# Optimization experiments

Measured on AMD Instinct MI355X. Metric: run time of the kernel, lower is better.

The kernel has to match this reference:

```python
import jax, jax.numpy as jnp
import numpy as np

DIM = 512
HEADS = 8
DIM_HEAD = 64
DIM_INNER = HEADS * DIM_HEAD
SCALE = DIM_HEAD ** -0.5


def setup_inputs() -> dict:
    key = jax.random.key(0)
    ks = jax.random.split(key, 8)
    b, n = 2, 1024
    x = jax.random.normal(ks[0], (b, n, DIM), dtype=jnp.float32)
    w = lambda k, i, o: jax.random.normal(k, (i, o), dtype=jnp.float32) * 0.02
    return {
        'x': x,
        'w_q_u': w(ks[1], DIM, DIM_INNER),
        'w_k_u': w(ks[2], DIM, DIM_INNER),
        'w_v_u': w(ks[3], DIM, DIM_INNER),
        'w_q_c': w(ks[4], DIM, DIM_INNER),
        'w_k_c': w(ks[5], DIM, DIM_INNER),
        'w_v_c': w(ks[6], DIM, DIM_INNER),
        'w_out': w(ks[7], DIM_INNER, DIM),
    }


def reference(x, w_q_u, w_k_u, w_v_u, w_q_c, w_k_c, w_v_c, w_out):
    b, n, _ = x.shape

    def proj(w):  # [b,n,dim] -> [b,h,n,d]
        return (x @ w).reshape(b, n, HEADS, DIM_HEAD).transpose(0, 2, 1, 3)

    q_u, k_u, v_u = proj(w_q_u), proj(w_k_u), proj(w_v_u)
    q_c, k_c, v_c = proj(w_q_c), proj(w_k_c), proj(w_v_c)

    idx = jnp.arange(n)
    causal = idx[:, None] >= idx[None, :]  # tril ones (binary causal mask)

    # term1 = (q_c @ v_u^T) * scale, zeroed above diagonal
    term1 = jnp.einsum('bhid,bhjd->bhij', q_c, v_u) * SCALE
    term1 = term1 * causal.astype(term1.dtype)

    # sigmoid term: (q_u @ k_u^T)*scale with lookahead mask tril(-inf, diag=0)
    logits_u = jnp.einsum('bhid,bhjd->bhij', q_u, k_u) * SCALE
    sig = jax.nn.sigmoid(jnp.where(causal, -jnp.inf, logits_u))

    # S_u[i,k] = sum_j term1[i,j] * sig[k,j]
    S_u = jnp.einsum('bhij,bhkj->bhik', term1, sig)

    # S_c: causal-masked QK
    S_c = jnp.einsum('bhid,bhjd->bhij', q_c, k_c) * SCALE
    S_c = jnp.where(causal, S_c, -jnp.inf)

    final_scores = S_c - jax.nn.silu(S_u)
    attn = jax.nn.softmax(final_scores, axis=-1)
    out = jnp.einsum('bhij,bhjd->bhid', attn, v_c)  # [b,h,n,d]
    out = out.transpose(0, 2, 1, 3).reshape(b, n, DIM_INNER)
    return out @ w_out
```

## Files before the change

kernel.cpp:

```cpp
#include <hip/hip_runtime.h>
#include <math.h>


typedef __bf16 bf16x8 __attribute__((ext_vector_type(8)));
typedef float f32x4 __attribute__((ext_vector_type(4)));

#define SCALE 0.125f

#define GLL(g, l) __builtin_amdgcn_global_load_lds(                         \
    (const __attribute__((address_space(1))) void*)(g),                     \
    (__attribute__((address_space(3))) void*)(l), 16, 0, 0)

__device__ __forceinline__ unsigned short f2bf(float f){
  unsigned int x = __builtin_bit_cast(unsigned int, f);
  unsigned int r = (x + 0x7fffu + ((x >> 16) & 1u)) >> 16;
  return (unsigned short)r;
}
__device__ __forceinline__ float bf2f(unsigned short u){
  unsigned int x = ((unsigned int)u) << 16;
  return __builtin_bit_cast(float, x);
}
__device__ __forceinline__ f32x4 mfma16(bf16x8 a, bf16x8 b, f32x4 c){
  return __builtin_amdgcn_mfma_f32_16x16x32_bf16(a, b, c, 0, 0, 0);
}
__device__ __forceinline__ bf16x8 ld8(const unsigned short* p){
  return *(const bf16x8*)p;
}

__device__ const unsigned char QK_CUM[16] =
  {0,1,2,4,6,9,12,16,20,25,30,36,42,49,56,64};

__device__ const unsigned char SC_RB[72] =
  {15,14,11,13,15,10,12,14,15,14,13,12,15,13,11, 9,
   12, 8, 6,15,13,11, 9, 7,15,13,14,10,14,12,10, 8,
    9, 3,14,12,10, 8, 6, 4,15,13,11, 7,11, 9, 7, 5,
   13,10, 8,11, 9, 6, 4, 2,15,14,12, 5, 7, 5, 3, 1,
   14,12,10, 8, 6, 4, 2, 0};
__device__ const unsigned char SC_CT[72] =
  { 1, 1, 0, 1, 2, 0, 1, 2, 0, 0, 0, 0, 3, 2, 1, 0,
    3, 1, 0, 4, 3, 2, 1, 0, 5, 4, 4, 2, 3, 2, 1, 0,
    3, 0, 5, 4, 3, 2, 1, 0, 6, 5, 4, 2, 3, 2, 1, 0,
    6, 4, 3, 5, 4, 2, 1, 0, 7, 6, 5, 1, 3, 2, 1, 0,
    7, 6, 5, 4, 3, 2, 1, 0};

__global__ __launch_bounds__(256) void k_prep(
    const float* __restrict__ x,
    const float* __restrict__ w0, const float* __restrict__ w1,
    const float* __restrict__ w2, const float* __restrict__ w3,
    const float* __restrict__ w4, const float* __restrict__ w5,
    const float* __restrict__ w6,
    unsigned short* __restrict__ xb, unsigned short* __restrict__ wT){
  int t = threadIdx.x;
  if (blockIdx.x < 576){
    for (int i = blockIdx.x * 256 + t; i < 262144; i += 576 * 256){
      float4 v = ((const float4*)x)[i];
      ushort4 o; o.x = f2bf(v.x); o.y = f2bf(v.y); o.z = f2bf(v.z); o.w = f2bf(v.w);
      ((ushort4*)xb)[i] = o;
    }
    return;
  }
  __shared__ float lds[64 * 65];
  int bx = blockIdx.x - 576;
  int mat = bx >> 6, tile = bx & 63, tr = tile >> 3, tc = tile & 7;
  int k0 = tr * 64, c0 = tc * 64;
  const float* src;
  switch (mat){
    case 0: src = w0; break; case 1: src = w1; break; case 2: src = w2; break;
    case 3: src = w3; break; case 4: src = w4; break; case 5: src = w5; break;
    default: src = w6; break;
  }
#pragma unroll
  for (int i = 0; i < 4; ++i){
    int r = (t >> 4) + i * 16, c4 = (t & 15) * 4;
    float4 v = *(const float4*)(src + (size_t)(k0 + r) * 512 + c0 + c4);
    lds[r * 65 + c4 + 0] = v.x; lds[r * 65 + c4 + 1] = v.y;
    lds[r * 65 + c4 + 2] = v.z; lds[r * 65 + c4 + 3] = v.w;
  }
  __syncthreads();
  unsigned short* dst = wT + (size_t)mat * 262144;
#pragma unroll
  for (int i = 0; i < 4; ++i){
    int oc = (t >> 4) + i * 16;
    int kq = (t & 15) * 4;
    ushort4 o;
    o.x = f2bf(lds[(kq + 0) * 65 + oc]);
    o.y = f2bf(lds[(kq + 1) * 65 + oc]);
    o.z = f2bf(lds[(kq + 2) * 65 + oc]);
    o.w = f2bf(lds[(kq + 3) * 65 + oc]);
    *(ushort4*)(dst + (size_t)(c0 + oc) * 512 + k0 + kq) = o;
  }
}

__global__ __launch_bounds__(256) void k_proj(
    const unsigned short* __restrict__ xb, const unsigned short* __restrict__ wT,
    unsigned short* __restrict__ P){
  __shared__ __align__(16) unsigned short sA[2 * 2 * 64 * 32];
  __shared__ __align__(16) unsigned short sB[2 * 2 * 128 * 32];
  int t = threadIdx.x, lane = t & 63, l16 = lane & 15, quad = lane >> 4;
  int w = t >> 6, wm = w >> 1, wn = w & 1;
  int bx = blockIdx.x;
  int mt = bx / 24, nt = bx - mt * 24;
  int M0 = mt * 64, N0 = nt * 128;
  int matb = N0 >> 9;
  int nin = N0 & 511;
  int srow = (lane >> 2), scol = (lane & 3) * 8;
  const unsigned short* gA = xb + (size_t)(M0 + w*16 + srow) * 512 + scol;
  const unsigned short* gB = wT + (size_t)matb * 262144
                               + (size_t)(nin + w*32 + srow) * 512 + scol;
  unsigned short* lA = sA + (w*16) * 32;
  unsigned short* lB = sB + (w*32) * 32;
  f32x4 acc[4][2] = {};
#define STAGE_PROJ(buf, k0) do {                                   \
    GLL(gA + (k0),               lA + (buf)*4096);                 \
    GLL(gB + (k0),               lB + (buf)*8192);                 \
    GLL(gB + (k0) + 16*512,      lB + (buf)*8192 + 16*32);         \
    GLL(gA + (k0) + 32,          lA + (buf)*4096 + 2048);          \
    GLL(gB + (k0) + 32,          lB + (buf)*8192 + 4096);          \
    GLL(gB + (k0) + 32 + 16*512, lB + (buf)*8192 + 4096 + 16*32);  \
  } while(0)
  STAGE_PROJ(0, 0);
  for (int it = 0; it < 8; ++it){
    if (it < 7){
      STAGE_PROJ((it+1) & 1, (it+1)*64);
      asm volatile("s_waitcnt vmcnt(6)" ::: "memory");
    } else {
      asm volatile("s_waitcnt vmcnt(0)" ::: "memory");
    }
    __builtin_amdgcn_s_barrier();
    int b = it & 1;
#pragma unroll
    for (int h = 0; h < 2; ++h){
      bf16x8 aw[4], ax[2];
#pragma unroll
      for (int fi = 0; fi < 4; ++fi)
        aw[fi] = *(const bf16x8*)(sB + b*8192 + h*4096 + (wn*64 + fi*16 + l16) * 32 + quad * 8);
#pragma unroll
      for (int mi = 0; mi < 2; ++mi)
        ax[mi] = *(const bf16x8*)(sA + b*4096 + h*2048 + (wm*32 + mi*16 + l16) * 32 + quad * 8);
#pragma unroll
      for (int fi = 0; fi < 4; ++fi)
#pragma unroll
        for (int mi = 0; mi < 2; ++mi)
          acc[fi][mi] = mfma16(aw[fi], ax[mi], acc[fi][mi]);
    }
    __builtin_amdgcn_s_barrier();
  }
#undef STAGE_PROJ
#pragma unroll
  for (int fi = 0; fi < 4; ++fi)
#pragma unroll
    for (int mi = 0; mi < 2; ++mi){
      int row = M0 + wm*32 + mi*16 + l16;
      int b_ = row >> 10, n_ = row & 1023;
      int c0 = N0 + wn*64 + fi*16 + quad*4;
      int h = (c0 & 511) >> 6, d = c0 & 63;
      int bh = b_*8 + h;
      ushort4 o;
      o.x = f2bf(acc[fi][mi][0]); o.y = f2bf(acc[fi][mi][1]);
      o.z = f2bf(acc[fi][mi][2]); o.w = f2bf(acc[fi][mi][3]);
      *(ushort4*)(P + (size_t)(matb*16 + bh) * 65536 + (size_t)n_ * 64 + d) = o;
    }
}

__global__ __launch_bounds__(256) void k_qk_vct(
    const unsigned short* __restrict__ P,
    unsigned short* __restrict__ term1, unsigned short* __restrict__ sig,
    unsigned short* __restrict__ vcT){
  int t = threadIdx.x;
  if (blockIdx.x < 256){
    __shared__ unsigned short lds[64 * 72];
    int bh = blockIdx.x >> 4, nt = blockIdx.x & 15;
    int N0 = nt * 64;
    const unsigned short* src = P + (size_t)(5*16 + bh) * 65536 + (size_t)N0 * 64;
#pragma unroll
    for (int i2 = 0; i2 < 2; ++i2){
      int id = i2 * 256 + t;
      int r = id >> 3, c8 = (id & 7) * 8;
      ushort4 v0 = *(const ushort4*)(src + r * 64 + c8);
      ushort4 v1 = *(const ushort4*)(src + r * 64 + c8 + 4);
      *(ushort4*)(lds + r * 72 + c8) = v0;
      *(ushort4*)(lds + r * 72 + c8 + 4) = v1;
    }
    __syncthreads();
    unsigned short* dst = vcT + (size_t)bh * 65536;
#pragma unroll
    for (int i2 = 0; i2 < 2; ++i2){
      int id = i2 * 256 + t;
      int dd = id >> 3, n8 = (id & 7) * 8;
      ushort4 a, b;
      a.x = lds[(n8+0)*72 + dd]; a.y = lds[(n8+1)*72 + dd];
      a.z = lds[(n8+2)*72 + dd]; a.w = lds[(n8+3)*72 + dd];
      b.x = lds[(n8+4)*72 + dd]; b.y = lds[(n8+5)*72 + dd];
      b.z = lds[(n8+6)*72 + dd]; b.w = lds[(n8+7)*72 + dd];
      *(ushort4*)(dst + (size_t)dd * 1024 + N0 + n8) = a;
      *(ushort4*)(dst + (size_t)dd * 1024 + N0 + n8 + 4) = b;
    }
    return;
  }
  __shared__ unsigned short sA[2 * 64 * 32], sB[2 * 128 * 32];
  int id = blockIdx.x - 256;
  int bh = id & 15, tt = id >> 4;
  int mat = (tt >= 72);
  int tl = mat ? tt - 72 : tt;
  int rb = 15;
  while (QK_CUM[rb] > tl) --rb;
  int ct = tl - QK_CUM[rb];
  int R0, C0;
  const unsigned short *Asrc, *Bsrc;
  if (!mat){ R0 = rb * 64;        C0 = ct * 128;
             Asrc = P + (size_t)(3*16 + bh) * 65536;
             Bsrc = P + (size_t)(2*16 + bh) * 65536; }
  else     { R0 = (15 - rb) * 64; C0 = (7 - ct) * 128;
             Asrc = P + (size_t)(0*16 + bh) * 65536;
             Bsrc = P + (size_t)(1*16 + bh) * 65536; }
  int lane = t & 63, l16 = lane & 15, quad = lane >> 4;
  int w = t >> 6, wm = w >> 1, wn = w & 1;
  int srow = lane >> 2, scol = (lane & 3) * 8;
  const unsigned short* gA = Asrc + (size_t)(R0 + w*16 + srow) * 64 + scol;
  const unsigned short* gB = Bsrc + (size_t)(C0 + w*32 + srow) * 64 + scol;
  unsigned short* lA0 = sA + (w*16) * 32;
  unsigned short* lB0 = sB + (w*32) * 32;
  unsigned short* lA1 = lA0 + 64 * 32;
  unsigned short* lB1 = lB0 + 128 * 32;
  f32x4 acc[4][2] = {};
  GLL(gA,              lA0);
  GLL(gB,              lB0);
  GLL(gB + 16*64,      lB0 + 16*32);
  GLL(gA + 32,         lA1);
  GLL(gB + 32,         lB1);
  GLL(gB + 32 + 16*64, lB1 + 16*32);
  __syncthreads();
#pragma unroll
  for (int h = 0; h < 2; ++h){
    bf16x8 af[2], bfr[4];
#pragma unroll
    for (int mi = 0; mi < 2; ++mi)
      af[mi] = *(const bf16x8*)(sA + h*2048 + (wm*32 + mi*16 + l16) * 32 + quad * 8);
#pragma unroll
    for (int fi = 0; fi < 4; ++fi)
      bfr[fi] = *(const bf16x8*)(sB + h*4096 + (wn*64 + fi*16 + l16) * 32 + quad * 8);
#pragma unroll
    for (int fi = 0; fi < 4; ++fi)
#pragma unroll
      for (int mi = 0; mi < 2; ++mi)
        acc[fi][mi] = mfma16(bfr[fi], af[mi], acc[fi][mi]);
  }
  unsigned short* out = (mat ? sig : term1) + (size_t)bh * 1048576;
#pragma unroll
  for (int fi = 0; fi < 4; ++fi)
#pragma unroll
    for (int mi = 0; mi < 2; ++mi){
      int row = R0 + wm*32 + mi*16 + l16;
      int c0 = C0 + wn*64 + fi*16 + quad*4;
      ushort4 o;
#pragma unroll
      for (int r = 0; r < 4; ++r){
        int col = c0 + r;
        float v = acc[fi][mi][r] * SCALE;
        unsigned short res;
        if (!mat) res = (col <= row) ? f2bf(v) : (unsigned short)0;
        else      res = (col >  row) ? f2bf(1.f / (1.f + expf(-v))) : (unsigned short)0;
        ((unsigned short*)&o)[r] = res;
      }
      *(ushort4*)(out + (size_t)row * 1024 + c0) = o;
    }
}

__global__ __launch_bounds__(256) void k_flash(
    const unsigned short* __restrict__ P,
    const unsigned short* __restrict__ term1,
    const unsigned short* __restrict__ sig,
    const unsigned short* __restrict__ vcT,
    float* __restrict__ Opart, float* __restrict__ MS){
  __shared__ __align__(16) unsigned short smem[2*64*32 + 2*128*32];
  unsigned short* sA = smem;
  unsigned short* sB = smem + 4096;
  unsigned short* probs = smem;
  float* red = (float*)smem;
  __shared__ float wpm[2][64], wps[2][64];
  int t = threadIdx.x;
  int bh = blockIdx.x & 15, tt = blockIdx.x >> 4;
  int rb = SC_RB[tt], ct = SC_CT[tt];
  int R0 = rb * 64, C0 = ct * 128;
  int n_it = rb + 1 - 2*ct;
  size_t sbase = (size_t)bh * 1048576;
  int lane = t & 63, l16 = lane & 15, quad = lane >> 4, w = t >> 6;
  int wm = w >> 1, wn = w & 1;
  int srow = lane >> 2, scol = (lane & 3) * 8;
  unsigned short* lA0 = sA + (w*16) * 32;
  unsigned short* lB0 = sB + (w*32) * 32;
  unsigned short* lA1 = lA0 + 2048;
  unsigned short* lB1 = lB0 + 4096;
  const unsigned short* Qc = P + (size_t)(3*16 + bh) * 65536;
  const unsigned short* Kc = P + (size_t)(4*16 + bh) * 65536;
  const unsigned short* Vt = vcT + (size_t)bh * 65536;
  const unsigned short* gA = term1 + sbase + (size_t)(R0 + w*16 + srow) * 1024 + scol;
  const unsigned short* gB = sig   + sbase + (size_t)(C0 + w*32 + srow) * 1024 + scol;
  f32x4 acc_u[4][2] = {};
  for (int it = 0; it < n_it; ++it){
    int j0 = C0 + it * 64;
    GLL(gA + j0,                lA0);
    GLL(gB + j0,                lB0);
    GLL(gB + j0 + 16*1024,      lB0 + 16*32);
    GLL(gA + j0 + 32,           lA1);
    GLL(gB + j0 + 32,           lB1);
    GLL(gB + j0 + 32 + 16*1024, lB1 + 16*32);
    __syncthreads();
#pragma unroll
    for (int h = 0; h < 2; ++h){
      bf16x8 af[2], bfr[4];
#pragma unroll
      for (int mi = 0; mi < 2; ++mi)
        af[mi] = *(const bf16x8*)(sA + h*2048 + (wm*32 + mi*16 + l16) * 32 + quad * 8);
#pragma unroll
      for (int fi = 0; fi < 4; ++fi)
        bfr[fi] = *(const bf16x8*)(sB + h*4096 + (wn*64 + fi*16 + l16) * 32 + quad * 8);
#pragma unroll
      for (int fi = 0; fi < 4; ++fi)
#pragma unroll
        for (int mi = 0; mi < 2; ++mi)
          acc_u[fi][mi] = mfma16(bfr[fi], af[mi], acc_u[fi][mi]);
    }
    __syncthreads();
  }
  f32x4 acc_c[4][2] = {};
#pragma unroll
  for (int kk = 0; kk < 2; ++kk){
    bf16x8 aqk[2], bfr[4];
#pragma unroll
    for (int mi = 0; mi < 2; ++mi)
      aqk[mi] = ld8(Qc + (size_t)(R0 + wm*32 + mi*16 + l16) * 64 + kk*32 + quad*8);
#pragma unroll
    for (int fi = 0; fi < 4; ++fi)
      bfr[fi] = ld8(Kc + (size_t)(C0 + wn*64 + fi*16 + l16) * 64 + kk*32 + quad*8);
#pragma unroll
    for (int fi = 0; fi < 4; ++fi)
#pragma unroll
      for (int mi = 0; mi < 2; ++mi)
        acc_c[fi][mi] = mfma16(bfr[fi], aqk[mi], acc_c[fi][mi]);
  }
  float pm0 = -INFINITY, pm1 = -INFINITY;
#pragma unroll
  for (int fi = 0; fi < 4; ++fi)
#pragma unroll
    for (int mi = 0; mi < 2; ++mi){
      int row = R0 + wm*32 + mi*16 + l16;
      int c0 = C0 + wn*64 + fi*16 + quad*4;
#pragma unroll
      for (int r = 0; r < 4; ++r){
        float su = acc_u[fi][mi][r];
        float s = acc_c[fi][mi][r] * SCALE - su / (1.f + expf(-su));
        if (c0 + r > row) s = -INFINITY;
        acc_u[fi][mi][r] = s;
        if (mi) pm1 = fmaxf(pm1, s); else pm0 = fmaxf(pm0, s);
      }
    }
  pm0 = fmaxf(pm0, __shfl_xor(pm0, 16)); pm0 = fmaxf(pm0, __shfl_xor(pm0, 32));
  pm1 = fmaxf(pm1, __shfl_xor(pm1, 16)); pm1 = fmaxf(pm1, __shfl_xor(pm1, 32));
  if (quad == 0){
    wpm[wn][wm*32 + l16]      = pm0;
    wpm[wn][wm*32 + 16 + l16] = pm1;
  }
  __syncthreads();
  float mr0 = fmaxf(wpm[0][wm*32 + l16],      wpm[1][wm*32 + l16]);
  float mr1 = fmaxf(wpm[0][wm*32 + 16 + l16], wpm[1][wm*32 + 16 + l16]);
  float ps0 = 0.f, ps1 = 0.f;
#pragma unroll
  for (int fi = 0; fi < 4; ++fi)
#pragma unroll
    for (int mi = 0; mi < 2; ++mi){
      ushort4 o;
#pragma unroll
      for (int r = 0; r < 4; ++r){
        float p = expf(acc_u[fi][mi][r] - (mi ? mr1 : mr0));
        if (mi) ps1 += p; else ps0 += p;
        ((unsigned short*)&o)[r] = f2bf(p);
      }
      *(ushort4*)(probs + (wm*32 + mi*16 + l16) * 136 + wn*64 + fi*16 + quad*4) = o;
    }
  ps0 += __shfl_xor(ps0, 16); ps0 += __shfl_xor(ps0, 32);
  ps1 += __shfl_xor(ps1, 16); ps1 += __shfl_xor(ps1, 32);
  if (quad == 0){
    wps[wn][wm*32 + l16]      = ps0;
    wps[wn][wm*32 + 16 + l16] = ps1;
  }
  __syncthreads();
  f32x4 acc_o[4] = {};
  const unsigned short* pr = probs + (16*w + l16) * 136 + quad * 8;
#pragma unroll
  for (int k0 = 0; k0 < 4; ++k0){
    bf16x8 a = *(const bf16x8*)(pr + k0*32);
#pragma unroll
    for (int fi = 0; fi < 4; ++fi){
      bf16x8 b = ld8(Vt + (size_t)(fi*16 + l16) * 1024 + C0 + k0*32 + quad*8);
      acc_o[fi] = mfma16(a, b, acc_o[fi]);
    }
  }
  __syncthreads();
#pragma unroll
  for (int fi = 0; fi < 4; ++fi)
#pragma unroll
    for (int r = 0; r < 4; ++r)
      red[(16*w + quad*4 + r) * 64 + fi*16 + l16] = acc_o[fi][r];
  __syncthreads();
  int slot = bh * 72 + QK_CUM[rb] + ct;
#pragma unroll
  for (int pass = 0; pass < 4; ++pass){
    int e = pass * 1024 + t * 4;
    *(float4*)(Opart + (size_t)slot * 4096 + e) = *(const float4*)(red + e);
  }
  if (t < 64){
    MS[(size_t)slot * 128 + t*2]     = fmaxf(wpm[0][t], wpm[1][t]);
    MS[(size_t)slot * 128 + t*2 + 1] = wps[0][t] + wps[1][t];
  }
}

__global__ __launch_bounds__(256) void k_comb(
    const float* __restrict__ Opart, const float* __restrict__ MS,
    unsigned short* __restrict__ O2){
  int t = threadIdx.x;
  int bh = blockIdx.x & 15, rb = blockIdx.x >> 4;
  int G = (rb >> 1) + 1;
  int r = t >> 2, cb = (t & 3) * 16;
  int base = bh * 72 + QK_CUM[rb];
  float m = -INFINITY;
#pragma unroll
  for (int g2 = 0; g2 < 8; ++g2)
    if (g2 < G) m = fmaxf(m, MS[(size_t)(base + g2) * 128 + r*2]);
  float wg[8]; float den = 0.f;
#pragma unroll
  for (int g2 = 0; g2 < 8; ++g2){
    if (g2 < G){
      wg[g2] = expf(MS[(size_t)(base + g2) * 128 + r*2] - m);
      den += MS[(size_t)(base + g2) * 128 + r*2 + 1] * wg[g2];
    } else wg[g2] = 0.f;
  }
  float inv = 1.f / den;
  int b_ = bh >> 3, h_ = bh & 7;
#pragma unroll
  for (int c4 = 0; c4 < 4; ++c4){
    float ax = 0.f, ay = 0.f, az = 0.f, aw = 0.f;
#pragma unroll
    for (int g2 = 0; g2 < 8; ++g2){
      if (g2 < G){
        float4 v = *(const float4*)(Opart + (size_t)(base + g2) * 4096 + r*64 + cb + c4*4);
        ax += v.x * wg[g2]; ay += v.y * wg[g2];
        az += v.z * wg[g2]; aw += v.w * wg[g2];
      }
    }
    ushort4 o;
    o.x = f2bf(ax * inv); o.y = f2bf(ay * inv);
    o.z = f2bf(az * inv); o.w = f2bf(aw * inv);
    *(ushort4*)(O2 + (size_t)(b_*1024 + rb*64 + r) * 512 + h_*64 + cb + c4*4) = o;
  }
}

__global__ __launch_bounds__(256) void k_out(
    const unsigned short* __restrict__ O2, const unsigned short* __restrict__ woT,
    float* __restrict__ out){
  __shared__ float red[4][1024];
  int t = threadIdx.x, lane = t & 63, l16 = lane & 15, quad = lane >> 4, w = t >> 6;
  int mt = blockIdx.x >> 3, nt = blockIdx.x & 7;
  int m0 = mt * 16, n0 = nt * 64;
  int r_ = m0 + l16;
  f32x4 acc[4] = {};
#pragma unroll
  for (int s = 0; s < 4; ++s){
    int kk = w * 128 + s * 32 + quad * 8;
    bf16x8 a = ld8(O2 + (size_t)r_ * 512 + kk);
#pragma unroll
    for (int fi = 0; fi < 4; ++fi){
      bf16x8 b = ld8(woT + (size_t)(n0 + fi*16 + l16) * 512 + kk);
      acc[fi] = mfma16(a, b, acc[fi]);
    }
  }
#pragma unroll
  for (int fi = 0; fi < 4; ++fi)
#pragma unroll
    for (int r = 0; r < 4; ++r)
      red[w][(quad*4 + r) * 64 + fi*16 + l16] = acc[fi][r];
  __syncthreads();
  float4 a0 = ((const float4*)red[0])[t];
  float4 a1 = ((const float4*)red[1])[t];
  float4 a2 = ((const float4*)red[2])[t];
  float4 a3 = ((const float4*)red[3])[t];
  float4 o;
  o.x = a0.x + a1.x + a2.x + a3.x;
  o.y = a0.y + a1.y + a2.y + a3.y;
  o.z = a0.z + a1.z + a2.z + a3.z;
  o.w = a0.w + a1.w + a2.w + a3.w;
  int e = t * 4, row = e >> 6, col = e & 63;
  *(float4*)(out + (size_t)(m0 + row) * 512 + n0 + col) = o;
}

extern "C" void kernel_launch(void* const* d_in, const int* in_sizes, int n_in,
                              void* d_out, int out_size, void* d_ws, size_t ws_size,
                              hipStream_t stream){
  const float* x = (const float*)d_in[0];
  float* out = (float*)d_out;
  unsigned short* ws = (unsigned short*)d_ws;

  unsigned short* wT    = ws;
  unsigned short* xb    = wT    + (size_t)7  * 262144;
  unsigned short* P     = xb    + (size_t)1048576;
  unsigned short* vcT   = P     + (size_t)96 * 65536;
  unsigned short* term1 = vcT   + (size_t)16 * 65536;
  unsigned short* sig   = term1 + (size_t)16 * 1048576;
  unsigned short* O2    = sig   + (size_t)16 * 1048576;
  unsigned short* fwsp  = O2    + (size_t)16 * 65536;
  float* Opart = (float*)fwsp;
  float* MS    = Opart + (size_t)1152 * 4096;

  k_prep<<<1024, 256, 0, stream>>>(
      x,
      (const float*)d_in[1], (const float*)d_in[2], (const float*)d_in[3],
      (const float*)d_in[4], (const float*)d_in[5], (const float*)d_in[6],
      (const float*)d_in[7], xb, wT);
  k_proj<<<768, 256, 0, stream>>>(xb, wT, P);
  k_qk_vct<<<2560, 256, 0, stream>>>(P, term1, sig, vcT);
  k_flash<<<1152, 256, 0, stream>>>(P, term1, sig, vcT, Opart, MS);
  k_comb<<<256, 256, 0, stream>>>(Opart, MS, O2);
  k_out<<<1024, 256, 0, stream>>>(O2, wT + (size_t)6 * 262144, out);
}
```

Measured before the change: 168.8 us.

## Enlarge flash tiles to 128x128 with 512 threads and XOR-swizzled LDS

Changes the S_u/flash kernel from 64x128 tiles with 256 threads to 128x128 tiles with 512 threads. This halves the number of tile blocks and the partial outputs the combine kernel has to merge, and lets each loaded sig tile be reused across more rows. The LDS staging layout is also switched to 64-wide rows with an XOR swizzle to avoid bank conflicts. In exchange there are fewer blocks (576) to fill the GPU and more per-block LDS and register pressure. The causal tile scheduling table is reordered.

```diff
diff --git a/kernel.cpp b/kernel.cpp
--- a/kernel.cpp
+++ b/kernel.cpp
@@ -30,18 +30,13 @@
 __device__ const unsigned char QK_CUM[16] =
   {0,1,2,4,6,9,12,16,20,25,30,36,42,49,56,64};
 
-__device__ const unsigned char SC_RB[72] =
-  {15,14,11,13,15,10,12,14,15,14,13,12,15,13,11, 9,
-   12, 8, 6,15,13,11, 9, 7,15,13,14,10,14,12,10, 8,
-    9, 3,14,12,10, 8, 6, 4,15,13,11, 7,11, 9, 7, 5,
-   13,10, 8,11, 9, 6, 4, 2,15,14,12, 5, 7, 5, 3, 1,
-   14,12,10, 8, 6, 4, 2, 0};
-__device__ const unsigned char SC_CT[72] =
-  { 1, 1, 0, 1, 2, 0, 1, 2, 0, 0, 0, 0, 3, 2, 1, 0,
-    3, 1, 0, 4, 3, 2, 1, 0, 5, 4, 4, 2, 3, 2, 1, 0,
-    3, 0, 5, 4, 3, 2, 1, 0, 6, 5, 4, 2, 3, 2, 1, 0,
-    6, 4, 3, 5, 4, 2, 1, 0, 7, 6, 5, 1, 3, 2, 1, 0,
-    7, 6, 5, 4, 3, 2, 1, 0};
+__device__ const unsigned char FL_RB2[36] =
+  {7, 7,6, 7,6,5, 7,6,5,4, 7,6,5,4,3, 7,6,5,4,3,2, 7,6,5,4,3,2,1,
+   7,6,5,4,3,2,1,0};
+__device__ const unsigned char FL_CT2[36] =
+  {0, 1,0, 2,1,0, 3,2,1,0, 4,3,2,1,0, 5,4,3,2,1,0, 6,5,4,3,2,1,0,
+   7,6,5,4,3,2,1,0};
+__device__ const unsigned char TRI2[8] = {0,1,3,6,10,15,21,28};
 
 __global__ __launch_bounds__(256) void k_prep(
     const float* __restrict__ x,
@@ -266,55 +261,56 @@
     }
 }
 
-__global__ __launch_bounds__(256) void k_flash(
+__global__ __launch_bounds__(512) void k_flash(
     const unsigned short* __restrict__ P,
     const unsigned short* __restrict__ term1,
     const unsigned short* __restrict__ sig,
     const unsigned short* __restrict__ vcT,
     float* __restrict__ Opart, float* __restrict__ MS){
-  __shared__ __align__(16) unsigned short smem[2*64*32 + 2*128*32];
+  __shared__ __align__(16) unsigned short smem[128 * 136];
   unsigned short* sA = smem;
-  unsigned short* sB = smem + 4096;
+  unsigned short* sB = smem + 8192;
   unsigned short* probs = smem;
   float* red = (float*)smem;
-  __shared__ float wpm[2][64], wps[2][64];
+  __shared__ float wpm[2][128], wps[2][128];
   int t = threadIdx.x;
-  int bh = blockIdx.x & 15, tt = blockIdx.x >> 4;
-  int rb = SC_RB[tt], ct = SC_CT[tt];
-  int R0 = rb * 64, C0 = ct * 128;
-  int n_it = rb + 1 - 2*ct;
+  int bh = blockIdx.x & 15, q = blockIdx.x >> 4;
+  int rb2 = FL_RB2[q], ct = FL_CT2[q];
+  int R0 = rb2 * 128, C0 = ct * 128;
+  int n_it = 2 * (rb2 + 1 - ct);
   size_t sbase = (size_t)bh * 1048576;
   int lane = t & 63, l16 = lane & 15, quad = lane >> 4, w = t >> 6;
   int wm = w >> 1, wn = w & 1;
-  int srow = lane >> 2, scol = (lane & 3) * 8;
-  unsigned short* lA0 = sA + (w*16) * 32;
-  unsigned short* lB0 = sB + (w*32) * 32;
-  unsigned short* lA1 = lA0 + 2048;
-  unsigned short* lB1 = lB0 + 4096;
+  int srow = lane >> 3;
+  int scol_sw = ((lane & 7) ^ srow) * 8;
   const unsigned short* Qc = P + (size_t)(3*16 + bh) * 65536;
   const unsigned short* Kc = P + (size_t)(4*16 + bh) * 65536;
   const unsigned short* Vt = vcT + (size_t)bh * 65536;
-  const unsigned short* gA = term1 + sbase + (size_t)(R0 + w*16 + srow) * 1024 + scol;
-  const unsigned short* gB = sig   + sbase + (size_t)(C0 + w*32 + srow) * 1024 + scol;
+  const unsigned short* gA = term1 + sbase + (size_t)(R0 + w*16 + srow) * 1024 + scol_sw;
+  const unsigned short* gB = sig   + sbase + (size_t)(C0 + w*16 + srow) * 1024 + scol_sw;
+  unsigned short* lA = sA + (w*16) * 64;
+  unsigned short* lB = sB + (w*16) * 64;
   f32x4 acc_u[4][2] = {};
   for (int it = 0; it < n_it; ++it){
     int j0 = C0 + it * 64;
-    GLL(gA + j0,                lA0);
-    GLL(gB + j0,                lB0);
-    GLL(gB + j0 + 16*1024,      lB0 + 16*32);
-    GLL(gA + j0 + 32,           lA1);
-    GLL(gB + j0 + 32,           lB1);
-    GLL(gB + j0 + 32 + 16*1024, lB1 + 16*32);
+    GLL(gA + j0,          lA);
+    GLL(gA + j0 + 8*1024, lA + 8*64);
+    GLL(gB + j0,          lB);
+    GLL(gB + j0 + 8*1024, lB + 8*64);
     __syncthreads();
 #pragma unroll
     for (int h = 0; h < 2; ++h){
       bf16x8 af[2], bfr[4];
 #pragma unroll
-      for (int mi = 0; mi < 2; ++mi)
-        af[mi] = *(const bf16x8*)(sA + h*2048 + (wm*32 + mi*16 + l16) * 32 + quad * 8);
-#pragma unroll
-      for (int fi = 0; fi < 4; ++fi)
-        bfr[fi] = *(const bf16x8*)(sB + h*4096 + (wn*64 + fi*16 + l16) * 32 + quad * 8);
+      for (int mi = 0; mi < 2; ++mi){
+        int row = wm*32 + mi*16 + l16;
+        af[mi] = *(const bf16x8*)(sA + row*64 + ((h*32 + quad*8) ^ ((row & 7) << 3)));
+      }
+#pragma unroll
+      for (int fi = 0; fi < 4; ++fi){
+        int row = wn*64 + fi*16 + l16;
+        bfr[fi] = *(const bf16x8*)(sB + row*64 + ((h*32 + quad*8) ^ ((row & 7) << 3)));
+      }
 #pragma unroll
       for (int fi = 0; fi < 4; ++fi)
 #pragma unroll
@@ -362,8 +358,10 @@
     wpm[wn][wm*32 + 16 + l16] = pm1;
   }
   __syncthreads();
-  float mr0 = fmaxf(wpm[0][wm*32 + l16],      wpm[1][wm*32 + l16]);
-  float mr1 = fmaxf(wpm[0][wm*32 + 16 + l16], wpm[1][wm*32 + 16 + l16]);
+  if (t < 128) wpm[0][t] = fmaxf(wpm[0][t], wpm[1][t]);
+  __syncthreads();
+  float mr0 = wpm[0][wm*32 + l16];
+  float mr1 = wpm[0][wm*32 + 16 + l16];
   float ps0 = 0.f, ps1 = 0.f;
 #pragma unroll
   for (int fi = 0; fi < 4; ++fi)
@@ -403,15 +401,15 @@
     for (int r = 0; r < 4; ++r)
       red[(16*w + quad*4 + r) * 64 + fi*16 + l16] = acc_o[fi][r];
   __syncthreads();
-  int slot = bh * 72 + QK_CUM[rb] + ct;
+  int slot = bh * 36 + TRI2[rb2] + ct;
 #pragma unroll
   for (int pass = 0; pass < 4; ++pass){
-    int e = pass * 1024 + t * 4;
-    *(float4*)(Opart + (size_t)slot * 4096 + e) = *(const float4*)(red + e);
-  }
-  if (t < 64){
-    MS[(size_t)slot * 128 + t*2]     = fmaxf(wpm[0][t], wpm[1][t]);
-    MS[(size_t)slot * 128 + t*2 + 1] = wps[0][t] + wps[1][t];
+    int e = pass * 2048 + t * 4;
+    *(float4*)(Opart + (size_t)slot * 8192 + e) = *(const float4*)(red + e);
+  }
+  if (t < 128){
+    MS[(size_t)slot * 256 + t*2]     = wpm[0][t];
+    MS[(size_t)slot * 256 + t*2 + 1] = wps[0][t] + wps[1][t];
   }
 }
 
@@ -419,31 +417,31 @@
     const float* __restrict__ Opart, const float* __restrict__ MS,
     unsigned short* __restrict__ O2){
   int t = threadIdx.x;
-  int bh = blockIdx.x & 15, rb = blockIdx.x >> 4;
-  int G = (rb >> 1) + 1;
-  int r = t >> 2, cb = (t & 3) * 16;
-  int base = bh * 72 + QK_CUM[rb];
+  int bh = blockIdx.x & 15, rb2 = blockIdx.x >> 4;
+  int G = rb2 + 1;
+  int r = t >> 1, cb = (t & 1) * 32;
+  int base = bh * 36 + TRI2[rb2];
   float m = -INFINITY;
 #pragma unroll
   for (int g2 = 0; g2 < 8; ++g2)
-    if (g2 < G) m = fmaxf(m, MS[(size_t)(base + g2) * 128 + r*2]);
+    if (g2 < G) m = fmaxf(m, MS[(size_t)(base + g2) * 256 + r*2]);
   float wg[8]; float den = 0.f;
 #pragma unroll
   for (int g2 = 0; g2 < 8; ++g2){
     if (g2 < G){
-      wg[g2] = expf(MS[(size_t)(base + g2) * 128 + r*2] - m);
-      den += MS[(size_t)(base + g2) * 128 + r*2 + 1] * wg[g2];
+      wg[g2] = expf(MS[(size_t)(base + g2) * 256 + r*2] - m);
+      den += MS[(size_t)(base + g2) * 256 + r*2 + 1] * wg[g2];
     } else wg[g2] = 0.f;
   }
   float inv = 1.f / den;
   int b_ = bh >> 3, h_ = bh & 7;
 #pragma unroll
-  for (int c4 = 0; c4 < 4; ++c4){
+  for (int c4 = 0; c4 < 8; ++c4){
     float ax = 0.f, ay = 0.f, az = 0.f, aw = 0.f;
 #pragma unroll
     for (int g2 = 0; g2 < 8; ++g2){
       if (g2 < G){
-        float4 v = *(const float4*)(Opart + (size_t)(base + g2) * 4096 + r*64 + cb + c4*4);
+        float4 v = *(const float4*)(Opart + (size_t)(base + g2) * 8192 + r*64 + cb + c4*4);
         ax += v.x * wg[g2]; ay += v.y * wg[g2];
         az += v.z * wg[g2]; aw += v.w * wg[g2];
       }
@@ -451,7 +449,7 @@
     ushort4 o;
     o.x = f2bf(ax * inv); o.y = f2bf(ay * inv);
     o.z = f2bf(az * inv); o.w = f2bf(aw * inv);
-    *(ushort4*)(O2 + (size_t)(b_*1024 + rb*64 + r) * 512 + h_*64 + cb + c4*4) = o;
+    *(ushort4*)(O2 + (size_t)(b_*1024 + rb2*128 + r) * 512 + h_*64 + cb + c4*4) = o;
   }
 }
 
@@ -509,7 +507,7 @@
   unsigned short* O2    = sig   + (size_t)16 * 1048576;
   unsigned short* fwsp  = O2    + (size_t)16 * 65536;
   float* Opart = (float*)fwsp;
-  float* MS    = Opart + (size_t)1152 * 4096;
+  float* MS    = Opart + (size_t)576 * 8192;
 
   k_prep<<<1024, 256, 0, stream>>>(
       x,
@@ -518,7 +516,7 @@
       (const float*)d_in[7], xb, wT);
   k_proj<<<768, 256, 0, stream>>>(xb, wT, P);
   k_qk_vct<<<2560, 256, 0, stream>>>(P, term1, sig, vcT);
-  k_flash<<<1152, 256, 0, stream>>>(P, term1, sig, vcT, Opart, MS);
-  k_comb<<<256, 256, 0, stream>>>(Opart, MS, O2);
+  k_flash<<<576, 512, 0, stream>>>(P, term1, sig, vcT, Opart, MS);
+  k_comb<<<128, 256, 0, stream>>>(Opart, MS, O2);
   k_out<<<1024, 256, 0, stream>>>(O2, wT + (size_t)6 * 262144, out);
 }
```

Result: slower. 181.8 us (+7.7%).
